# Optimization experiments

Measured on AMD Instinct MI355X. Metric: run time of the kernel, lower is better.

## Reference

```python
import jax, jax.numpy as jnp
import numpy as np

N_HEAD = 16
COND_LEN = 256  # n_unmasked; mask[i, j] == 1 iff j < COND_LEN + i


def rotate_half(x):
    # interleaved pairs: (x0, x1, x2, x3, ...) -> (-x1, x0, -x3, x2, ...)
    x = x.reshape(x.shape[:-1] + (-1, 2))
    x1, x2 = x[..., 0], x[..., 1]
    return jnp.stack([-x2, x1], axis=-1).reshape(x.shape[:-2] + (-1,))


def apply_rotary_pos_emb(t, freqs):
    # t: [B, H, T, l], freqs: [T, l] -> broadcast over B, H
    return t * jnp.cos(freqs) + rotate_half(t) * jnp.sin(freqs)


def setup_inputs() -> dict:
    key = jax.random.key(0)
    ks = jax.random.split(key, 12)
    B, T, C = 8, 769, 1024
    l = 32
    s = 0.02
    return {
        "x_q": jax.random.normal(ks[0], (B, T, C), jnp.float32),
        "x_kv": jax.random.normal(ks[1], (B, T, C), jnp.float32),
        "rotary_pos_emb": jax.random.uniform(ks[2], (T, l), jnp.float32),
        "Wq": jax.random.normal(ks[3], (C, C), jnp.float32) * s,
        "bq": jnp.zeros((C,), jnp.float32),
        "Wk": jax.random.normal(ks[4], (C, C), jnp.float32) * s,
        "bk": jnp.zeros((C,), jnp.float32),
        "Wv": jax.random.normal(ks[5], (C, C), jnp.float32) * s,
        "bv": jnp.zeros((C,), jnp.float32),
        "Wp": jax.random.normal(ks[6], (C, C), jnp.float32) * s,
        "bp": jnp.zeros((C,), jnp.float32),
    }


def reference(x_q, x_kv, rotary_pos_emb, Wq, bq, Wk, bk, Wv, bv, Wp, bp):
    B, T_q, C = x_q.shape
    T_kv = x_kv.shape[1]
    H = N_HEAD
    hd = C // H

    def heads(x, W, b, T):
        return (x @ W.T + b).reshape(B, T, H, hd).transpose(0, 2, 1, 3)  # [B,H,T,hd]

    q = heads(x_q, Wq, bq, T_q)
    k = heads(x_kv, Wk, bk, T_kv)
    v = heads(x_kv, Wv, bv, T_kv)

    # partial rotary on first l dims of q and k
    l = rotary_pos_emb.shape[-1]
    q = jnp.concatenate([apply_rotary_pos_emb(q[..., :l], rotary_pos_emb), q[..., l:]], axis=-1)
    k = jnp.concatenate([apply_rotary_pos_emb(k[..., :l], rotary_pos_emb), k[..., l:]], axis=-1)

    att = jnp.einsum("bhqd,bhkd->bhqk", q, k) * (1.0 / jnp.sqrt(jnp.asarray(hd, q.dtype)))
    # custom prefix+causal mask: allowed iff col < COND_LEN + row
    row = jnp.arange(T_q)[:, None]
    col = jnp.arange(T_kv)[None, :]
    allowed = col < (COND_LEN + row)  # [T_q, T_kv]
    att = jnp.where(allowed[None, None], att, -jnp.inf)
    att = jax.nn.softmax(att, axis=-1)

    y = jnp.einsum("bhqk,bhkd->bhqd", att, v)
    y = y.transpose(0, 2, 1, 3).reshape(B, T_q, C)
    return y @ Wp.T + bp
```

## Files before the change

kernel.cpp:

```cpp
#include <hip/hip_runtime.h>
#include <stdint.h>

#define B_    8
#define T_    769
#define C_    1024
#define H_    16
#define COND_ 256
#define NTOK  (B_*T_)
#define BH_   (B_*H_)
#define TP_   896

typedef short    v8s  __attribute__((ext_vector_type(8)));
typedef float    v4f  __attribute__((ext_vector_type(4)));
typedef uint16_t u16x4 __attribute__((ext_vector_type(4)));
typedef uint16_t u16x8 __attribute__((ext_vector_type(8)));
typedef uint32_t u32x4 __attribute__((ext_vector_type(4)));

__device__ __forceinline__ uint16_t f2bf(float f) {
  uint32_t u = __builtin_bit_cast(uint32_t, f);
  u += 0x7fffu + ((u >> 16) & 1u);
  return (uint16_t)(u >> 16);
}
__device__ __forceinline__ float bf2f(uint16_t h) {
  uint32_t u = ((uint32_t)h) << 16;
  return __builtin_bit_cast(float, u);
}

__device__ __forceinline__ void gl_lds16(const void* gptr, void* lptr) {
  __builtin_amdgcn_global_load_lds(
      (const __attribute__((address_space(1))) uint32_t*)gptr,
      (__attribute__((address_space(3))) uint32_t*)lptr,
      16, 0, 0);
}

__device__ __forceinline__ int xcd_swz_bij(int orig, int nwg) {
  int q = nwg >> 3, r = nwg & 7;
  int xcd = orig & 7;
  int base = (xcd < r) ? xcd * (q + 1) : r * (q + 1) + (xcd - r) * q;
  return base + (orig >> 3);
}

__global__ __launch_bounds__(256) void convert_bf16(
    const float* xq, const float* xkv, const float* wq, const float* wk,
    const float* wv, const float* wp,
    uint16_t* dxq, uint16_t* dxkv, uint16_t* dwq, uint16_t* dwk,
    uint16_t* dwv, uint16_t* dwp)
{
  int bid = blockIdx.x;
  const float* s; uint16_t* d; int base;
  if (bid < 6152)       { s = xq;  d = dxq;  base = bid; }
  else if (bid < 12304) { s = xkv; d = dxkv; base = bid - 6152; }
  else {
    int r = bid - 12304;
    int wsel = r >> 10; base = r & 1023;
    s = (wsel == 0) ? wq : (wsel == 1) ? wk : (wsel == 2) ? wv : wp;
    d = (wsel == 0) ? dwq : (wsel == 1) ? dwk : (wsel == 2) ? dwv : dwp;
  }
  int i = base * 256 + threadIdx.x;
  float4 f = ((const float4*)s)[i];
  u16x4 o;
  o[0] = f2bf(f.x); o[1] = f2bf(f.y); o[2] = f2bf(f.z); o[3] = f2bf(f.w);
  ((u16x4*)d)[i] = o;
}


__device__ __forceinline__ void gemm_stage64(
    const uint16_t* const Aptr[4], const uint16_t* const Bptr[4],
    int k0, uint16_t* sA, uint16_t* sB, int tid)
{
  #pragma unroll
  for (int r = 0; r < 4; r++) {
    gl_lds16(Aptr[r] + k0, sA + (r * 256 + tid) * 8);
    gl_lds16(Bptr[r] + k0, sB + (r * 256 + tid) * 8);
  }
}

__device__ __forceinline__ void gemm_compute64(
    const uint16_t* sAc, const uint16_t* sBc, v4f acc[4][4],
    int rbase, int cbase, int quad, int l15)
{
  #pragma unroll
  for (int s = 0; s < 2; s++) {
    v8s af[4], bfv[4];
    #pragma unroll
    for (int i = 0; i < 4; i++) {
      int m = rbase + i * 16 + l15;
      af[i] = *(const v8s*)(sAc + m * 64 + (((s * 4 + quad) ^ (m & 7)) * 8));
    }
    #pragma unroll
    for (int j = 0; j < 4; j++) {
      int n = cbase + j * 16 + l15;
      bfv[j] = *(const v8s*)(sBc + n * 64 + (((s * 4 + quad) ^ (n & 7)) * 8));
    }
    #pragma unroll
    for (int i = 0; i < 4; i++)
      #pragma unroll
      for (int j = 0; j < 4; j++)
        acc[i][j] = __builtin_amdgcn_mfma_f32_16x16x32_bf16(af[i], bfv[j], acc[i][j], 0, 0, 0);
  }
}

__device__ __forceinline__ void gemm_mainloop64(
    const uint16_t* A, const uint16_t* W, int M, int row0, int col0,
    v4f acc[4][4], uint16_t* sA, uint16_t* sB)
{
  const int tid = threadIdx.x;
  const int lane = tid & 63, w = tid >> 6, quad = lane >> 4, l15 = lane & 15;
  const int rbase = (w >> 1) * 64, cbase = (w & 1) * 64;

  const uint16_t* Aptr[4];
  const uint16_t* Bptr[4];
  #pragma unroll
  for (int r = 0; r < 4; r++) {
    int c = r * 256 + tid;
    int row = c >> 3, qp = c & 7;
    int g = qp ^ (row & 7);
    Aptr[r] = A + (size_t)min(row0 + row, M - 1) * 1024 + g * 8;
    Bptr[r] = W + (size_t)(col0 + row) * 1024 + g * 8;
  }

  #pragma unroll
  for (int i = 0; i < 4; i++)
    #pragma unroll
    for (int j = 0; j < 4; j++) acc[i][j] = (v4f)0.0f;

  uint16_t* sA0 = sA;         uint16_t* sB0 = sB;
  uint16_t* sA1 = sA + 8192;  uint16_t* sB1 = sB + 8192;

  gemm_stage64(Aptr, Bptr, 0,  sA0, sB0, tid);
  gemm_stage64(Aptr, Bptr, 64, sA1, sB1, tid);

  #pragma unroll 1
  for (int t = 0; t < 16; t++) {
    if (t < 15) {
      asm volatile("s_waitcnt vmcnt(8)" ::: "memory");
    } else {
      asm volatile("s_waitcnt vmcnt(0)" ::: "memory");
    }
    __builtin_amdgcn_s_barrier();
    asm volatile("" ::: "memory");
    uint16_t* cA = (t & 1) ? sA1 : sA0;
    uint16_t* cB = (t & 1) ? sB1 : sB0;
    gemm_compute64(cA, cB, acc, rbase, cbase, quad, l15);
    asm volatile("s_waitcnt lgkmcnt(0)" ::: "memory");
    __builtin_amdgcn_s_barrier();
    asm volatile("" ::: "memory");
    if (t + 2 < 16)
      gemm_stage64(Aptr, Bptr, (t + 2) * 64, cA, cB, tid);
  }
}

__global__ __launch_bounds__(256) void gemm_qkv(
    const uint16_t* xq, const uint16_t* xkv, const uint16_t* Wqkv,
    const float* bq, const float* bk, const float* bv, const float* freqs,
    uint16_t* Q, uint16_t* K, uint16_t* V)
{
  __shared__ uint16_t sA[2 * 128 * 64];
  __shared__ uint16_t sB[2 * 128 * 64];
  const int swz = xcd_swz_bij(blockIdx.x, 1176);
  const int ct = swz % 24, rt = swz / 24;
  const int z = ct >> 3;
  const int col0 = ct * 128, row0 = rt * 128;
  const uint16_t* A = (z == 0) ? xq : xkv;
  const float* bias  = (z == 0) ? bq : (z == 1 ? bk : bv);
  uint16_t* dst      = (z == 0) ? Q  : (z == 1 ? K  : V);

  v4f acc[4][4];
  gemm_mainloop64(A, Wqkv, NTOK, row0, col0, acc, sA, sB);

  const int tid = threadIdx.x;
  const int lane = tid & 63, w = tid >> 6, quad = lane >> 4, l15 = lane & 15;
  const int rbase = (w >> 1) * 64, cbase = (w & 1) * 64;
  #pragma unroll
  for (int i = 0; i < 4; i++) {
    #pragma unroll
    for (int reg = 0; reg < 4; reg++) {
      int n = row0 + rbase + i * 16 + quad * 4 + reg;
      bool ok = (n < NTOK);
      int nn = min(n, NTOK - 1);
      int b = nn / T_, t = nn % T_;
      float vj[4];
      #pragma unroll
      for (int j = 0; j < 4; j++)
        vj[j] = acc[i][j][reg] + bias[(col0 + cbase + j * 16 + l15) & 1023];
      if (z < 2) {
        float v0 = vj[0], v1 = vj[1];
        float p0 = __shfl_xor(v0, 1);
        float p1 = __shfl_xor(v1, 1);
        float f0 = freqs[t * 32 + l15];
        float f1 = freqs[t * 32 + 16 + l15];
        float s0, c0, s1, c1;
        __sincosf(f0, &s0, &c0);
        __sincosf(f1, &s1, &c1);
        if (l15 & 1) { vj[0] = v0 * c0 + p0 * s0; vj[1] = v1 * c1 + p1 * s1; }
        else         { vj[0] = v0 * c0 - p0 * s0; vj[1] = v1 * c1 - p1 * s1; }
      }
      if (z == 0) {
        #pragma unroll
        for (int j = 0; j < 4; j++) vj[j] *= 0.125f;
      }
      if (ok) {
        #pragma unroll
        for (int j = 0; j < 4; j++) {
          int col = col0 + cbase + j * 16 + l15;
          int h = (col >> 6) & 15, d = col & 63;
          dst[((size_t)(b * H_ + h) * T_ + t) * 64 + d] = f2bf(vj[j]);
        }
      }
    }
  }
}

__global__ __launch_bounds__(256) void gemm_out(
    const uint16_t* Y, const uint16_t* wp, const float* bp, float* out)
{
  __shared__ uint16_t sA[2 * 128 * 64];
  __shared__ uint16_t sB[2 * 128 * 64];
  const int swz = xcd_swz_bij(blockIdx.x, 392);
  const int ct = swz & 7, rt = swz >> 3;
  const int col0 = ct * 128, row0 = rt * 128;
  v4f acc[4][4];
  gemm_mainloop64(Y, wp, NTOK, row0, col0, acc, sA, sB);

  const int tid = threadIdx.x;
  const int lane = tid & 63, w = tid >> 6, quad = lane >> 4, l15 = lane & 15;
  const int rbase = (w >> 1) * 64, cbase = (w & 1) * 64;
  #pragma unroll
  for (int i = 0; i < 4; i++) {
    #pragma unroll
    for (int reg = 0; reg < 4; reg++) {
      int n = row0 + rbase + i * 16 + quad * 4 + reg;
      if (n < NTOK) {
        #pragma unroll
        for (int j = 0; j < 4; j++) {
          int col = col0 + cbase + j * 16 + l15;
          out[(size_t)n * 1024 + col] = acc[i][j][reg] + bp[col];
        }
      }
    }
  }
}

__global__ __launch_bounds__(256) void transpose_v(const uint16_t* Vb, uint16_t* Vt)
{
  __shared__ uint16_t sT[64 * 64];
  const int tid = threadIdx.x;
  const int t0 = blockIdx.x * 64, bh = blockIdx.y;
  const uint16_t* src = Vb + (size_t)bh * T_ * 64;
  #pragma unroll
  for (int r = 0; r < 2; r++) {
    int task = r * 256 + tid;
    int t = task >> 3, oc = task & 7;
    int gt = min(t0 + t, T_ - 1);
    u16x8 v = *(const u16x8*)(src + (size_t)gt * 64 + oc * 8);
    int p = oc ^ (t & 7) ^ ((t >> 3) & 7);
    *(u16x8*)(sT + t * 64 + p * 8) = v;
  }
  __syncthreads();
  uint16_t* dst = Vt + (size_t)bh * 64 * TP_;
  #pragma unroll
  for (int r = 0; r < 2; r++) {
    int task = r * 256 + tid;
    int o = task & 7, d = task >> 3;
    u16x8 v;
    #pragma unroll
    for (int k = 0; k < 8; k++) {
      int t = o * 8 + k;
      int p = (d >> 3) ^ k ^ o;
      v[k] = sT[t * 64 + p * 8 + (d & 7)];
    }
    *(u16x8*)(dst + (size_t)d * TP_ + t0 + o * 8) = v;
  }
}

__global__ __launch_bounds__(256) void attn(
    const uint16_t* Q, const uint16_t* K, const uint16_t* Vt, uint16_t* Y)
{
  __shared__ uint16_t sK[128 * 64];
  __shared__ uint16_t sVT[64 * 128];

  const int tid = threadIdx.x;
  const int lane = tid & 63, w = tid >> 6, quad = lane >> 4, l15 = lane & 15;
  const int swz = xcd_swz_bij(blockIdx.x, 1664);
  const int qt = swz % 13, bh = swz / 13;
  const int b = bh >> 4, h = bh & 15;
  const int q0 = qt * 64;

  const uint16_t* Qb = Q + (size_t)bh * T_ * 64;
  const uint16_t* Kb = K + (size_t)bh * T_ * 64;
  const uint16_t* Vtb = Vt + (size_t)bh * 64 * TP_;

  const int qa = q0 + w * 16 + l15;
  const int lim = min(COND_ + qa, T_);
  const int qr = min(qa, T_ - 1);
  v8s aq0 = *(const v8s*)(Qb + (size_t)qr * 64 + quad * 8);
  v8s aq1 = *(const v8s*)(Qb + (size_t)qr * 64 + 32 + quad * 8);

  float l_r = 0.f;
  v4f o[4];
  #pragma unroll
  for (int r = 0; r < 4; r++) o[r] = (v4f)0.0f;

  const int kend = min(T_, q0 + 319);
  const int nkt = (kend + 127) >> 7;

  const int srcA = (((quad << 1)    ) & 3) * 16 + l15;
  const int srcB = (((quad << 1) + 1) & 3) * 16 + l15;
  const bool hiq = (quad >= 2);

  #define STAGE_K(K0)                                                     \
    {                                                                     \
      _Pragma("unroll")                                                   \
      for (int r = 0; r < 4; r++) {                                       \
        int c = r * 256 + tid;                                            \
        int key = c >> 3, qp = c & 7;                                     \
        int g = qp ^ (key & 7);                                           \
        int gk = min((K0) + key, T_ - 1);                                 \
        gl_lds16(Kb + (size_t)gk * 64 + g * 8, sK + c * 8);               \
      }                                                                   \
    }
  #define STAGE_V(K0)                                                     \
    {                                                                     \
      _Pragma("unroll")                                                   \
      for (int r = 0; r < 4; r++) {                                       \
        int c = r * 256 + tid;                                            \
        int d = c >> 4, p = c & 15;                                       \
        int g = (p & 8) | ((p ^ d) & 7);                                  \
        gl_lds16(Vtb + (size_t)d * TP_ + (K0) + g * 8, sVT + c * 8);      \
      }                                                                   \
    }

  STAGE_K(0);
  STAGE_V(0);

  for (int kt = 0; kt < nkt; kt++) {
    const int k0 = kt * 128;
    asm volatile("s_waitcnt vmcnt(4)" ::: "memory");
    __builtin_amdgcn_s_barrier();
    asm volatile("" ::: "memory");

    v4f s[8];
    #pragma unroll
    for (int cb = 0; cb < 8; cb++) {
      int key_l = cb * 16 + l15;
      v8s b0 = *(const v8s*)(sK + (key_l * 8 + ((quad) ^ (key_l & 7))) * 8);
      v8s b1 = *(const v8s*)(sK + (key_l * 8 + ((4 + quad) ^ (key_l & 7))) * 8);
      v4f zz = (v4f)0.0f;
      zz = __builtin_amdgcn_mfma_f32_16x16x32_bf16(b0, aq0, zz, 0, 0, 0);
      zz = __builtin_amdgcn_mfma_f32_16x16x32_bf16(b1, aq1, zz, 0, 0, 0);
      s[cb] = zz;
    }

    uint32_t pk01[8], pk23[8];
    float rs = 0.f;
    const bool full = (k0 + 128 <= COND_ + q0) && (k0 + 128 <= T_);
    if (full) {
      #pragma unroll
      for (int cb = 0; cb < 8; cb++) {
        uint16_t pb0 = f2bf(__expf(s[cb][0]));
        uint16_t pb1 = f2bf(__expf(s[cb][1]));
        uint16_t pb2 = f2bf(__expf(s[cb][2]));
        uint16_t pb3 = f2bf(__expf(s[cb][3]));
        pk01[cb] = (uint32_t)pb0 | ((uint32_t)pb1 << 16);
        pk23[cb] = (uint32_t)pb2 | ((uint32_t)pb3 << 16);
        rs += bf2f(pb0) + bf2f(pb1) + bf2f(pb2) + bf2f(pb3);
      }
    } else {
      #pragma unroll
      for (int cb = 0; cb < 8; cb++) {
        int keyb = k0 + cb * 16 + quad * 4;
        float p0 = (keyb + 0 < lim) ? __expf(s[cb][0]) : 0.f;
        float p1 = (keyb + 1 < lim) ? __expf(s[cb][1]) : 0.f;
        float p2 = (keyb + 2 < lim) ? __expf(s[cb][2]) : 0.f;
        float p3 = (keyb + 3 < lim) ? __expf(s[cb][3]) : 0.f;
        uint16_t pb0 = f2bf(p0), pb1 = f2bf(p1), pb2 = f2bf(p2), pb3 = f2bf(p3);
        pk01[cb] = (uint32_t)pb0 | ((uint32_t)pb1 << 16);
        pk23[cb] = (uint32_t)pb2 | ((uint32_t)pb3 << 16);
        rs += bf2f(pb0) + bf2f(pb1) + bf2f(pb2) + bf2f(pb3);
      }
    }
    rs += __shfl_xor(rs, 16);
    rs += __shfl_xor(rs, 32);
    l_r += rs;

    asm volatile("s_waitcnt vmcnt(0)" ::: "memory");
    __builtin_amdgcn_s_barrier();
    asm volatile("" ::: "memory");
    if (kt + 1 < nkt) STAGE_K(k0 + 128);

    #pragma unroll
    for (int ks = 0; ks < 4; ks++) {
      const int cbE = 2 * ks, cbO = 2 * ks + 1;
      uint32_t a01E = __shfl((int)pk01[cbE], srcA), a01O = __shfl((int)pk01[cbO], srcA);
      uint32_t a23E = __shfl((int)pk23[cbE], srcA), a23O = __shfl((int)pk23[cbO], srcA);
      uint32_t b01E = __shfl((int)pk01[cbE], srcB), b01O = __shfl((int)pk01[cbO], srcB);
      uint32_t b23E = __shfl((int)pk23[cbE], srcB), b23O = __shfl((int)pk23[cbO], srcB);
      u32x4 pw;
      pw[0] = hiq ? a01O : a01E;
      pw[1] = hiq ? a23O : a23E;
      pw[2] = hiq ? b01O : b01E;
      pw[3] = hiq ? b23O : b23E;
      v8s ap = __builtin_bit_cast(v8s, pw);
      #pragma unroll
      for (int cbd = 0; cbd < 4; cbd++) {
        int d = cbd * 16 + l15;
        v8s bv = *(const v8s*)(sVT + d * 128 + (((ks * 4 + quad) ^ (d & 7)) * 8));
        o[cbd] = __builtin_amdgcn_mfma_f32_16x16x32_bf16(ap, bv, o[cbd], 0, 0, 0);
      }
    }

    asm volatile("s_waitcnt lgkmcnt(0)" ::: "memory");
    __builtin_amdgcn_s_barrier();
    asm volatile("" ::: "memory");
    if (kt + 1 < nkt) STAGE_V(k0 + 128);
  }
  #undef STAGE_K
  #undef STAGE_V

  #pragma unroll
  for (int reg = 0; reg < 4; reg++) {
    int r_ = quad * 4 + reg;
    float lv = __shfl(l_r, (lane & 48) | r_);
    int t = q0 + w * 16 + r_;
    if (t < T_) {
      float inv = 1.0f / lv;
      #pragma unroll
      for (int cbd = 0; cbd < 4; cbd++) {
        int d = cbd * 16 + l15;
        Y[((size_t)(b * T_ + t)) * C_ + h * 64 + d] = f2bf(o[cbd][reg] * inv);
      }
    }
  }
}

extern "C" void kernel_launch(void* const* d_in, const int* in_sizes, int n_in,
                              void* d_out, int out_size, void* d_ws, size_t ws_size,
                              hipStream_t stream)
{
  const float* x_q   = (const float*)d_in[0];
  const float* x_kv  = (const float*)d_in[1];
  const float* freqs = (const float*)d_in[2];
  const float* Wq = (const float*)d_in[3];
  const float* bq = (const float*)d_in[4];
  const float* Wk = (const float*)d_in[5];
  const float* bk = (const float*)d_in[6];
  const float* Wv = (const float*)d_in[7];
  const float* bv = (const float*)d_in[8];
  const float* Wp = (const float*)d_in[9];
  const float* bp = (const float*)d_in[10];
  float* out = (float*)d_out;

  const size_t SZX = (size_t)NTOK * C_;
  const size_t SZW = (size_t)C_ * C_;
  uint16_t* ws = (uint16_t*)d_ws;
  uint16_t* xq_bf  = ws;
  uint16_t* xkv_bf = xq_bf + SZX;
  uint16_t* wq_bf  = xkv_bf + SZX;
  uint16_t* wk_bf  = wq_bf + SZW;
  uint16_t* wv_bf  = wk_bf + SZW;
  uint16_t* wp_bf  = wv_bf + SZW;
  uint16_t* Qb = wp_bf + SZW;
  uint16_t* Kb = Qb + SZX;
  uint16_t* Vb = Kb + SZX;
  uint16_t* Vt = ws;
  uint16_t* Yb = Vb;

  convert_bf16<<<dim3(16400), 256, 0, stream>>>(
      x_q, x_kv, Wq, Wk, Wv, Wp, xq_bf, xkv_bf, wq_bf, wk_bf, wv_bf, wp_bf);

  gemm_qkv<<<dim3(1176), 256, 0, stream>>>(
      xq_bf, xkv_bf, wq_bf, bq, bk, bv, freqs, Qb, Kb, Vb);

  transpose_v<<<dim3(13, BH_), 256, 0, stream>>>(Vb, Vt);

  attn<<<dim3(1664), 256, 0, stream>>>(Qb, Kb, Vt, Yb);

  gemm_out<<<dim3(392), 256, 0, stream>>>(Yb, wp_bf, bp, out);
}
```

Before: 277.9 us.

## Rewrite QKV GEMM with 256x256 tiles, 8 waves and swizzled LDS

Replaces the 128x128, 4-wave QKV projection GEMM with a 256x256 tile computed by 512 threads (8 waves). Each wave owns a 128x64 output block, the K step drops to 32, and A/B loads into LDS are split around the two MFMA halves for finer-grained overlap. LDS rows use an XOR swizzle to avoid bank conflicts, and MFMA bursts are wrapped in s_setprio. The intent is more data reuse per LDS byte and fewer global loads. The trade-off is only 300 blocks on 256 CUs, which leaves a partial second wave and more padding waste on the last row tile.

```diff
diff --git a/kernel.cpp b/kernel.cpp
--- a/kernel.cpp
+++ b/kernel.cpp
@@ -63,6 +63,159 @@
   ((u16x4*)d)[i] = o;
 }
 
+
+__device__ __forceinline__ int swz4(int m, int c) {
+  return c ^ (m & 3) ^ ((m >> 2) & 3);
+}
+
+struct QOff { int a0[4]; int a1[4]; int b[4]; };
+
+template<int VMC, bool STG>
+__device__ __forceinline__ void ktile2(
+    const uint16_t* cA, const uint16_t* cB, uint16_t* nA, uint16_t* nB,
+    int knext,
+    const uint16_t* ga0, const uint16_t* ga1,
+    const uint16_t* gb0, const uint16_t* gb1,
+    int tid, QOff off, v4f (&acc)[8][4])
+{
+  if (STG) {
+    gl_lds16(ga0 + knext, nA + tid * 8);
+    gl_lds16(ga1 + knext, nA + 4096 + tid * 8);
+  }
+  asm volatile("s_waitcnt vmcnt(%0)" :: "n"(VMC) : "memory");
+  __builtin_amdgcn_s_barrier();
+  asm volatile("" ::: "memory");
+  v8s a[4], b[4];
+  #pragma unroll
+  for (int i = 0; i < 4; i++) a[i] = *(const v8s*)(cA + off.a0[i]);
+  #pragma unroll
+  for (int j = 0; j < 4; j++) b[j] = *(const v8s*)(cB + off.b[j]);
+  __builtin_amdgcn_s_setprio(1);
+  #pragma unroll
+  for (int i = 0; i < 4; i++)
+    #pragma unroll
+    for (int j = 0; j < 4; j++)
+      acc[i][j] = __builtin_amdgcn_mfma_f32_16x16x32_bf16(a[i], b[j], acc[i][j], 0, 0, 0);
+  __builtin_amdgcn_s_setprio(0);
+  if (STG) {
+    gl_lds16(gb0 + knext, nB + tid * 8);
+    gl_lds16(gb1 + knext, nB + 4096 + tid * 8);
+  }
+  v8s a2[4];
+  #pragma unroll
+  for (int i = 0; i < 4; i++) a2[i] = *(const v8s*)(cA + off.a1[i]);
+  asm volatile("s_waitcnt lgkmcnt(0)" ::: "memory");
+  __builtin_amdgcn_s_barrier();
+  asm volatile("" ::: "memory");
+  __builtin_amdgcn_s_setprio(1);
+  #pragma unroll
+  for (int i = 0; i < 4; i++)
+    #pragma unroll
+    for (int j = 0; j < 4; j++)
+      acc[4 + i][j] = __builtin_amdgcn_mfma_f32_16x16x32_bf16(a2[i], b[j], acc[4 + i][j], 0, 0, 0);
+  __builtin_amdgcn_s_setprio(0);
+}
+
+__global__ __launch_bounds__(512, 2) void gemm_qkv(
+    const uint16_t* xq, const uint16_t* xkv, const uint16_t* Wqkv,
+    const float* bq, const float* bk, const float* bv, const float* freqs,
+    uint16_t* Q, uint16_t* K, uint16_t* V)
+{
+  __shared__ uint16_t sA[2][8192];
+  __shared__ uint16_t sB[2][8192];
+
+  const int tid = threadIdx.x;
+  const int lane = tid & 63, wid = tid >> 6, quad = (lane >> 4), l15 = lane & 15;
+  const int wr = wid >> 2, wc = wid & 3;
+
+  const int swz = xcd_swz_bij(blockIdx.x, 300);
+  const int ct = swz % 12, rt = swz / 12;
+  const int z = ct >> 2;
+  const int col0 = ct * 256, row0 = rt * 256;
+  const uint16_t* A = (z == 0) ? xq : xkv;
+  const float* bias  = (z == 0) ? bq : (z == 1 ? bk : bv);
+  uint16_t* dst      = (z == 0) ? Q  : (z == 1 ? K  : V);
+
+  const int ms = tid >> 2, sl = tid & 3;
+  const int c0 = swz4(ms, sl);
+  const uint16_t* ga0 = A + (size_t)min(row0 + ms,       NTOK - 1) * 1024 + c0 * 8;
+  const uint16_t* ga1 = A + (size_t)min(row0 + 128 + ms, NTOK - 1) * 1024 + c0 * 8;
+  const uint16_t* gb0 = Wqkv + (size_t)(col0 + ms) * 1024 + c0 * 8;
+  const uint16_t* gb1 = Wqkv + (size_t)(col0 + 128 + ms) * 1024 + c0 * 8;
+
+  QOff off;
+  #pragma unroll
+  for (int i = 0; i < 4; i++) {
+    int m0 = wr * 128 + i * 16 + l15;
+    int m1 = m0 + 64;
+    off.a0[i] = m0 * 32 + swz4(m0, quad) * 8;
+    off.a1[i] = m1 * 32 + swz4(m1, quad) * 8;
+    int n = wc * 64 + i * 16 + l15;
+    off.b[i] = n * 32 + swz4(n, quad) * 8;
+  }
+
+  v4f acc[8][4];
+  #pragma unroll
+  for (int i = 0; i < 8; i++)
+    #pragma unroll
+    for (int j = 0; j < 4; j++) acc[i][j] = (v4f)0.0f;
+
+  gl_lds16(ga0, sA[0] + tid * 8);
+  gl_lds16(ga1, sA[0] + 4096 + tid * 8);
+  gl_lds16(gb0, sB[0] + tid * 8);
+  gl_lds16(gb1, sB[0] + 4096 + tid * 8);
+
+  #pragma unroll 1
+  for (int t = 0; t < 30; t += 2) {
+    ktile2<2, true>(sA[0], sB[0], sA[1], sB[1], (t + 1) * 32,
+                    ga0, ga1, gb0, gb1, tid, off, acc);
+    ktile2<2, true>(sA[1], sB[1], sA[0], sB[0], (t + 2) * 32,
+                    ga0, ga1, gb0, gb1, tid, off, acc);
+  }
+  ktile2<2, true >(sA[0], sB[0], sA[1], sB[1], 31 * 32,
+                   ga0, ga1, gb0, gb1, tid, off, acc);
+  ktile2<0, false>(sA[1], sB[1], sA[0], sB[0], 0,
+                   ga0, ga1, gb0, gb1, tid, off, acc);
+
+  #pragma unroll
+  for (int fr = 0; fr < 8; fr++) {
+    #pragma unroll
+    for (int reg = 0; reg < 4; reg++) {
+      int n = row0 + wr * 128 + (fr >> 2) * 64 + (fr & 3) * 16 + quad * 4 + reg;
+      bool ok = (n < NTOK);
+      int nn = min(n, NTOK - 1);
+      int b = nn / T_, t = nn % T_;
+      float vj[4];
+      #pragma unroll
+      for (int j = 0; j < 4; j++)
+        vj[j] = acc[fr][j][reg] + bias[(col0 + wc * 64 + j * 16 + l15) & 1023];
+      if (z < 2) {
+        float v0 = vj[0], v1 = vj[1];
+        float p0 = __shfl_xor(v0, 1);
+        float p1 = __shfl_xor(v1, 1);
+        float f0 = freqs[t * 32 + l15];
+        float f1 = freqs[t * 32 + 16 + l15];
+        float s0, c0_, s1, c1;
+        __sincosf(f0, &s0, &c0_);
+        __sincosf(f1, &s1, &c1);
+        if (l15 & 1) { vj[0] = v0 * c0_ + p0 * s0; vj[1] = v1 * c1 + p1 * s1; }
+        else         { vj[0] = v0 * c0_ - p0 * s0; vj[1] = v1 * c1 - p1 * s1; }
+      }
+      if (z == 0) {
+        #pragma unroll
+        for (int j = 0; j < 4; j++) vj[j] *= 0.125f;
+      }
+      if (ok) {
+        #pragma unroll
+        for (int j = 0; j < 4; j++) {
+          int col = col0 + wc * 64 + j * 16 + l15;
+          int h = (col >> 6) & 15, d = col & 63;
+          dst[((size_t)(b * H_ + h) * T_ + t) * 64 + d] = f2bf(vj[j]);
+        }
+      }
+    }
+  }
+}
 
 __device__ __forceinline__ void gemm_stage64(
     const uint16_t* const Aptr[4], const uint16_t* const Bptr[4],
@@ -147,67 +300,6 @@
     asm volatile("" ::: "memory");
     if (t + 2 < 16)
       gemm_stage64(Aptr, Bptr, (t + 2) * 64, cA, cB, tid);
-  }
-}
-
-__global__ __launch_bounds__(256) void gemm_qkv(
-    const uint16_t* xq, const uint16_t* xkv, const uint16_t* Wqkv,
-    const float* bq, const float* bk, const float* bv, const float* freqs,
-    uint16_t* Q, uint16_t* K, uint16_t* V)
-{
-  __shared__ uint16_t sA[2 * 128 * 64];
-  __shared__ uint16_t sB[2 * 128 * 64];
-  const int swz = xcd_swz_bij(blockIdx.x, 1176);
-  const int ct = swz % 24, rt = swz / 24;
-  const int z = ct >> 3;
-  const int col0 = ct * 128, row0 = rt * 128;
-  const uint16_t* A = (z == 0) ? xq : xkv;
-  const float* bias  = (z == 0) ? bq : (z == 1 ? bk : bv);
-  uint16_t* dst      = (z == 0) ? Q  : (z == 1 ? K  : V);
-
-  v4f acc[4][4];
-  gemm_mainloop64(A, Wqkv, NTOK, row0, col0, acc, sA, sB);
-
-  const int tid = threadIdx.x;
-  const int lane = tid & 63, w = tid >> 6, quad = lane >> 4, l15 = lane & 15;
-  const int rbase = (w >> 1) * 64, cbase = (w & 1) * 64;
-  #pragma unroll
-  for (int i = 0; i < 4; i++) {
-    #pragma unroll
-    for (int reg = 0; reg < 4; reg++) {
-      int n = row0 + rbase + i * 16 + quad * 4 + reg;
-      bool ok = (n < NTOK);
-      int nn = min(n, NTOK - 1);
-      int b = nn / T_, t = nn % T_;
-      float vj[4];
-      #pragma unroll
-      for (int j = 0; j < 4; j++)
-        vj[j] = acc[i][j][reg] + bias[(col0 + cbase + j * 16 + l15) & 1023];
-      if (z < 2) {
-        float v0 = vj[0], v1 = vj[1];
-        float p0 = __shfl_xor(v0, 1);
-        float p1 = __shfl_xor(v1, 1);
-        float f0 = freqs[t * 32 + l15];
-        float f1 = freqs[t * 32 + 16 + l15];
-        float s0, c0, s1, c1;
-        __sincosf(f0, &s0, &c0);
-        __sincosf(f1, &s1, &c1);
-        if (l15 & 1) { vj[0] = v0 * c0 + p0 * s0; vj[1] = v1 * c1 + p1 * s1; }
-        else         { vj[0] = v0 * c0 - p0 * s0; vj[1] = v1 * c1 - p1 * s1; }
-      }
-      if (z == 0) {
-        #pragma unroll
-        for (int j = 0; j < 4; j++) vj[j] *= 0.125f;
-      }
-      if (ok) {
-        #pragma unroll
-        for (int j = 0; j < 4; j++) {
-          int col = col0 + cbase + j * 16 + l15;
-          int h = (col >> 6) & 15, d = col & 63;
-          dst[((size_t)(b * H_ + h) * T_ + t) * 64 + d] = f2bf(vj[j]);
-        }
-      }
-    }
   }
 }
 
@@ -468,7 +560,7 @@
   convert_bf16<<<dim3(16400), 256, 0, stream>>>(
       x_q, x_kv, Wq, Wk, Wv, Wp, xq_bf, xkv_bf, wq_bf, wk_bf, wv_bf, wp_bf);
 
-  gemm_qkv<<<dim3(1176), 256, 0, stream>>>(
+  gemm_qkv<<<dim3(300), 512, 0, stream>>>(
       xq_bf, xkv_bf, wq_bf, bq, bk, bv, freqs, Qb, Kb, Vb);
 
   transpose_v<<<dim3(13, BH_), 256, 0, stream>>>(Vb, Vt);
```

Result: no change. 277.1 us (-0.3%).
